# Performance work log

Measured on AMD Instinct MI355X. Metric: run time of the kernel, lower is better.

## Reference

```python
import jax, jax.numpy as jnp
import numpy as np

B, S, D = 2, 1024, 4096          # batch, prefill seqlen, model dim
H, KVH, HD = 32, 8, 128          # q heads, kv heads, head dim
MAX = 2048                       # kv-cache capacity
THETA = 1000000.0
REP = H // KVH


def _rope_tables(pos):
    # pos: [S] int -> cos/sin [S, HD]
    inv_freq = 1.0 / (THETA ** (jnp.arange(0, HD, 2, dtype=jnp.float32) / HD))
    freqs = pos[:, None].astype(jnp.float32) * inv_freq[None, :]
    emb = jnp.concatenate([freqs, freqs], axis=-1)
    return jnp.cos(emb), jnp.sin(emb)


def _rotate_half(t):
    t1, t2 = jnp.split(t, 2, axis=-1)
    return jnp.concatenate([-t2, t1], axis=-1)


def setup_inputs() -> dict:
    key = jax.random.key(0)
    k = jax.random.split(key, 8)
    sc = 1.0 / np.sqrt(D)
    x = jax.random.normal(k[0], (B, S, D), jnp.float32)
    storage_idx = jnp.arange(S, dtype=jnp.int32)
    cache = jnp.zeros((2, 1, B, KVH, MAX, HD), jnp.float32)
    causal = jnp.tril(jnp.ones((MAX, MAX), bool))
    mask = jnp.where(causal, 0.0, -1e9).astype(jnp.float32)
    Wq = jax.random.normal(k[1], (D, H * HD), jnp.float32) * sc
    bq = jax.random.normal(k[2], (H * HD,), jnp.float32) * 0.01
    Wk = jax.random.normal(k[3], (D, KVH * HD), jnp.float32) * sc
    bk = jax.random.normal(k[4], (KVH * HD,), jnp.float32) * 0.01
    Wv = jax.random.normal(k[5], (D, KVH * HD), jnp.float32) * sc
    bv = jax.random.normal(k[6], (KVH * HD,), jnp.float32) * 0.01
    Wo = jax.random.normal(k[7], (H * HD, D), jnp.float32) * sc
    return {"x": x, "storage_idx": storage_idx, "cache": cache, "mask": mask,
            "Wq": Wq, "bq": bq, "Wk": Wk, "bk": bk, "Wv": Wv, "bv": bv, "Wo": Wo}


def reference(x, storage_idx, cache, mask, Wq, bq, Wk, bk, Wv, bv, Wo):
    bsz, seqlen, _ = x.shape
    # QKV projections -> [b, heads, s, hd]
    xq = (x @ Wq + bq).reshape(bsz, seqlen, H, HD).transpose(0, 2, 1, 3)
    xk = (x @ Wk + bk).reshape(bsz, seqlen, KVH, HD).transpose(0, 2, 1, 3)
    xv = (x @ Wv + bv).reshape(bsz, seqlen, KVH, HD).transpose(0, 2, 1, 3)
    # inline RoPE at positions storage_idx
    cos, sin = _rope_tables(storage_idx)       # [s, hd]
    cos = cos[None, None]                      # [1,1,s,hd]
    sin = sin[None, None]
    xq = xq * cos + _rotate_half(xq) * sin
    xk = xk * cos + _rotate_half(xk) * sin
    # KV-cache scatter (index_copy_ on dim -2 at storage_idx)
    keys = cache[0, 0].at[:, :, storage_idx, :].set(xk)    # [b, kvh, MAX, hd]
    values = cache[1, 0].at[:, :, storage_idx, :].set(xv)
    # GQA: repeat kv heads
    keys = jnp.repeat(keys, REP, axis=1)       # [b, H, MAX, hd]
    values = jnp.repeat(values, REP, axis=1)
    # attention with additive mask rows gathered at storage_idx
    scores = jnp.einsum('bhqd,bhkd->bhqk', xq, keys) / np.sqrt(HD)
    scores = scores + mask[storage_idx][None, None]        # [b, H, s, MAX]
    attn = jax.nn.softmax(scores, axis=-1)
    out = jnp.einsum('bhqk,bhkd->bhqd', attn, values)
    out = out.transpose(0, 2, 1, 3).reshape(bsz, seqlen, H * HD)
    return out @ Wo
```

## Files before the change

kernel.cpp:

```cpp
#include <hip/hip_runtime.h>
#include <hip/hip_bf16.h>

typedef unsigned short u16;
typedef unsigned int   u32;
using bf16x8 = __attribute__((ext_vector_type(8))) short;
using f32x4  = __attribute__((ext_vector_type(4))) float;
using f32x16 = __attribute__((ext_vector_type(16))) float;

#define AS1 __attribute__((address_space(1)))
#define AS3 __attribute__((address_space(3)))

static constexpr int S_   = 1024;
static constexpr int D_   = 4096;
static constexpr int H_   = 32;
static constexpr int KVH_ = 8;
static constexpr int HD_  = 128;
static constexpr int NQKV = H_*HD_ + 2*KVH_*HD_;

__device__ __forceinline__ u16 f2bf(float f) {
  union { float f; u32 u; } v; v.f = f;
  u32 r = v.u + 0x7FFFu + ((v.u >> 16) & 1u);
  return (u16)(r >> 16);
}

__global__ void k_convert(const float* __restrict__ src, u16* __restrict__ dst, int n4) {
  int i = blockIdx.x * blockDim.x + threadIdx.x;
  if (i >= n4) return;
  float4 v = ((const float4*)src)[i];
  ushort4 o;
  o.x = f2bf(v.x); o.y = f2bf(v.y); o.z = f2bf(v.z); o.w = f2bf(v.w);
  ((ushort4*)dst)[i] = o;
}

__global__ __launch_bounds__(256) void k_transpose_all(
    const float* __restrict__ Wq, const float* __restrict__ Wk,
    const float* __restrict__ Wv, const float* __restrict__ Wo,
    u16* __restrict__ WB, u16* __restrict__ WoT) {
  constexpr int K = 4096;
  __shared__ float t[64][65];
  int id = blockIdx.x;
  const float* src; u16* dst; int N, tx, ty;
  if (id < 4096)      { src = Wq; dst = WB;                        N = 4096; tx = id & 63; ty = id >> 6; }
  else if (id < 5120) { id -= 4096; src = Wk; dst = WB + (size_t)4096*K; N = 1024; tx = id & 15; ty = id >> 4; }
  else if (id < 6144) { id -= 5120; src = Wv; dst = WB + (size_t)5120*K; N = 1024; tx = id & 15; ty = id >> 4; }
  else                { id -= 6144; src = Wo; dst = WoT;           N = 4096; tx = id & 63; ty = id >> 6; }
  int k0 = ty * 64, n0 = tx * 64;
  int tid = threadIdx.x;
  int lr = tid >> 4;
  int lc = (tid & 15) * 4;
#pragma unroll
  for (int i = 0; i < 4; ++i) {
    float4 v = *(const float4*)&src[(size_t)(k0 + lr + i*16) * N + n0 + lc];
    t[lc+0][lr + i*16] = v.x;
    t[lc+1][lr + i*16] = v.y;
    t[lc+2][lr + i*16] = v.z;
    t[lc+3][lr + i*16] = v.w;
  }
  __syncthreads();
  int wn = tid >> 3;
  int wk = (tid & 7) * 8;
#pragma unroll
  for (int i = 0; i < 2; ++i) {
    const float* row = &t[wn + i*32][wk];
    ushort4 a, b;
    a.x = f2bf(row[0]); a.y = f2bf(row[1]); a.z = f2bf(row[2]); a.w = f2bf(row[3]);
    b.x = f2bf(row[4]); b.y = f2bf(row[5]); b.z = f2bf(row[6]); b.w = f2bf(row[7]);
    u16* o = &dst[(size_t)(n0 + wn + i*32) * K + k0 + wk];
    *(ushort4*)o = a;
    *(ushort4*)(o + 4) = b;
  }
}

__global__ void k_transpose_v(const u16* __restrict__ src, u16* __restrict__ dst) {
  __shared__ u16 t[32][33];
  int bg = blockIdx.z;
  int s0 = blockIdx.x * 32, h0 = blockIdx.y * 32;
  src += (size_t)bg * S_ * HD_;
  dst += (size_t)bg * S_ * HD_;
  int tx = threadIdx.x, ty = threadIdx.y;
#pragma unroll
  for (int i = 0; i < 4; ++i)
    t[ty + i*8][tx] = src[(size_t)(s0 + ty + i*8) * HD_ + h0 + tx];
  __syncthreads();
#pragma unroll
  for (int i = 0; i < 4; ++i)
    dst[(size_t)(h0 + ty + i*8) * S_ + s0 + tx] = t[tx][ty + i*8];
}

__global__ void k_rope(const int* __restrict__ sidx, float* __restrict__ cosd,
                       float* __restrict__ sind) {
  int i = blockIdx.x * blockDim.x + threadIdx.x;
  int s = i >> 6, d = i & 63;
  float pos  = (float)sidx[s];
  float invf = expf(-0.21586735246819178f * (float)d);
  float ph   = pos * invf;
  cosd[i] = cosf(ph);
  sind[i] = sinf(ph);
}

#define BAR   __builtin_amdgcn_s_barrier()
#define SCHB  __builtin_amdgcn_sched_barrier(0)

__global__ __launch_bounds__(512, 2) void k_gemmq(
    const u16* __restrict__ A, const u16* __restrict__ Bt,
    const float* __restrict__ bq, const float* __restrict__ bk,
    const float* __restrict__ bv,
    const float* __restrict__ cosd, const float* __restrict__ sind,
    u16* __restrict__ qb, u16* __restrict__ kb, u16* __restrict__ vb)
{
  constexpr int K = 4096;
  constexpr int ABYT = 256*128, BBYT = 256*128, STEP = ABYT+BBYT;
  __shared__ __align__(16) char lds[2*STEP];

  const int cpx = (int)gridDim.x >> 3;
  const int wkid = ((int)blockIdx.x & 7)*cpx + ((int)blockIdx.x >> 3);
  const int NT = 24;
  const int m0 = (wkid / NT) * 256, n0 = (wkid % NT) * 256;
  const int tid = threadIdx.x, w = tid>>6, lane = tid&63;
  const int l15 = lane&15, l4 = lane>>4;
  const int wr = w>>1, wc = w&1;
  const int row0 = tid>>3;
  const int ss = (tid&7) ^ (row0&7);
  const int NK = K >> 6;

  f32x4 acc[4][8];
#pragma unroll
  for (int i = 0; i < 4; ++i)
#pragma unroll
    for (int j = 0; j < 8; ++j) acc[i][j] = (f32x4){0.f,0.f,0.f,0.f};

  bf16x8 af[2][2][2];
  bf16x8 bfr[2][4][2];

#define QCHUNK(kt_, part_, r0c_)                                              \
  __builtin_amdgcn_global_load_lds(                                           \
    (AS1 void*)(((part_) ? Bt + (size_t)(n0 + (r0c_) + row0)*K                \
                         : A  + (size_t)(m0 + (r0c_) + row0)*K)               \
                + (size_t)(kt_)*64 + ss*8),                                   \
    (AS3 void*)(lds + ((kt_)&1)*STEP + (part_)*ABYT + (r0c_)*128 + w*1024),   \
    16, 0, 0)

#define QR_A(mh_, lA_)                                                        \
  _Pragma("unroll") for (int i2 = 0; i2 < 2; ++i2)                            \
  _Pragma("unroll") for (int kk = 0; kk < 2; ++kk) {                          \
    int row = wr*64 + ((mh_)*2 + i2)*16 + l15;                                \
    af[mh_][i2][kk] = *(const bf16x8*)((lA_) + row*128 + (((kk*4+l4) ^ (row&7)) << 4)); }

#define QR_B(nh_, lB_)                                                        \
  _Pragma("unroll") for (int jj = 0; jj < 4; ++jj)                            \
  _Pragma("unroll") for (int kk = 0; kk < 2; ++kk) {                          \
    int row = wc*128 + ((nh_)*4 + jj)*16 + l15;                               \
    bfr[nh_][jj][kk] = *(const bf16x8*)((lB_) + row*128 + (((kk*4+l4) ^ (row&7)) << 4)); }

#define QMFMA(mh_, nh_)                                                       \
  __builtin_amdgcn_s_setprio(1);                                              \
  _Pragma("unroll") for (int i2 = 0; i2 < 2; ++i2)                            \
  _Pragma("unroll") for (int jj = 0; jj < 4; ++jj)                            \
  _Pragma("unroll") for (int kk = 0; kk < 2; ++kk)                            \
    acc[(mh_)*2+i2][(nh_)*4+jj] = __builtin_amdgcn_mfma_f32_16x16x32_bf16(    \
        af[mh_][i2][kk], bfr[nh_][jj][kk], acc[(mh_)*2+i2][(nh_)*4+jj], 0, 0, 0); \
  __builtin_amdgcn_s_setprio(0);

  QCHUNK(0,0,0); QCHUNK(0,0,64); QCHUNK(0,0,128); QCHUNK(0,0,192);
  QCHUNK(0,1,0); QCHUNK(0,1,64); QCHUNK(0,1,128); QCHUNK(0,1,192);
  QCHUNK(1,0,0); QCHUNK(1,0,64); QCHUNK(1,0,128); QCHUNK(1,0,192);
  QCHUNK(1,1,0); QCHUNK(1,1,64); QCHUNK(1,1,128); QCHUNK(1,1,192);
  asm volatile("s_waitcnt vmcnt(8)" ::: "memory");
  BAR; SCHB;
  {
    const char* lA0 = lds;
    const char* lB0 = lds + ABYT;
    QR_A(0, lA0); QR_B(0, lB0);
  }

  for (int kt = 0; kt < NK; ++kt) {
    const char* lA = lds + (kt&1)*STEP;
    const char* lB = lA + ABYT;
    QR_B(1, lB);
    asm volatile("s_waitcnt lgkmcnt(8)" ::: "memory");
    SCHB;
    QMFMA(0,0);
    QR_A(1, lA);
    asm volatile("s_waitcnt lgkmcnt(4)" ::: "memory");
    BAR; SCHB;
    if (kt+2 < NK) { QCHUNK(kt+2,1,0); QCHUNK(kt+2,1,64); QCHUNK(kt+2,1,128); QCHUNK(kt+2,1,192); }
    QMFMA(0,1);
    asm volatile("s_waitcnt lgkmcnt(0)" ::: "memory");
    BAR; SCHB;
    if (kt+2 < NK) { QCHUNK(kt+2,0,0); QCHUNK(kt+2,0,64); QCHUNK(kt+2,0,128); QCHUNK(kt+2,0,192); }
    QMFMA(1,0);
    if (kt+1 < NK) {
      if (kt+2 < NK) asm volatile("s_waitcnt vmcnt(8)" ::: "memory");
      else           asm volatile("s_waitcnt vmcnt(0)" ::: "memory");
      BAR; SCHB;
      const char* lAn = lds + ((kt+1)&1)*STEP;
      const char* lBn = lAn + ABYT;
      QR_A(0, lAn); QR_B(0, lBn);
      SCHB;
    }
    QMFMA(1,1);
  }
#undef QCHUNK
#undef QR_A
#undef QR_B
#undef QMFMA

  const int btype = (n0 >= H_*HD_) + (n0 >= H_*HD_ + KVH_*HD_);
  const int colbase = n0 + wc*128 - (btype==1 ? H_*HD_ : btype==2 ? H_*HD_+KVH_*HD_ : 0);
  const int hloc = colbase >> 7;
  const float* bias = btype==0 ? bq : btype==1 ? bk : bv;
  u16* dst = btype==0 ? qb : btype==1 ? kb : vb;
  const int nheads = btype==0 ? H_ : KVH_;
  const float scale = btype==0 ? 0.08838834764831845f : 1.0f;

  float bb[8];
#pragma unroll
  for (int j = 0; j < 8; ++j) bb[j] = bias[colbase + j*16 + l15];

#pragma unroll
  for (int i = 0; i < 4; ++i)
#pragma unroll
    for (int r = 0; r < 4; ++r) {
      int sr = m0 + wr*64 + i*16 + l4*4 + r;
      int b_ = sr >> 10, s_ = sr & 1023;
      size_t obase = (((size_t)b_*nheads + hloc)*S_ + s_)*(size_t)HD_;
      if (btype < 2) {
#pragma unroll
        for (int j = 0; j < 4; ++j) {
          float cs = cosd[s_*64 + j*16 + l15];
          float sn = sind[s_*64 + j*16 + l15];
          float lo = acc[i][j][r]   + bb[j];
          float hi = acc[i][j+4][r] + bb[j+4];
          dst[obase + j*16 + l15]      = f2bf((lo*cs - hi*sn) * scale);
          dst[obase + 64 + j*16 + l15] = f2bf((hi*cs + lo*sn) * scale);
        }
      } else {
#pragma unroll
        for (int j = 0; j < 8; ++j)
          dst[obase + j*16 + l15] = f2bf(acc[i][j][r] + bb[j]);
      }
    }
}

__global__ __launch_bounds__(512, 2) void k_gemmo(
    const u16* __restrict__ A, const u16* __restrict__ Bt,
    float* __restrict__ C, int N, int K)
{
  constexpr int ABYT = 128*128, BBYT = 256*128, STEP = ABYT+BBYT;
  __shared__ __align__(16) char lds[2*STEP];

  const int cpx = (int)gridDim.x >> 3;
  const int wkid = ((int)blockIdx.x & 7)*cpx + ((int)blockIdx.x >> 3);
  const int NT = N / 256;
  const int m0 = (wkid / NT) * 128, n0 = (wkid % NT) * 256;
  const int tid = threadIdx.x, w = tid>>6, lane = tid&63;
  const int l31 = lane & 31, lh = lane >> 5;
  const int wr = w>>2, wc = w&3;
  const int row0 = tid>>3;
  const int ss = (tid&7) ^ (row0&7);
  const int NK = K >> 6;

  f32x16 acc00 = {}, acc01 = {}, acc10 = {}, acc11 = {};

  bf16x8 af[2][4];
  bf16x8 bfr[2][4];

#define OCHUNK(kt_, part_, r0c_)                                              \
  __builtin_amdgcn_global_load_lds(                                           \
    (AS1 void*)(((part_) ? Bt + (size_t)(n0 + (r0c_) + row0)*K                \
                         : A  + (size_t)(m0 + (r0c_) + row0)*K)               \
                + (size_t)(kt_)*64 + ss*8),                                   \
    (AS3 void*)(lds + ((kt_)&1)*STEP + (part_)*ABYT + (r0c_)*128 + w*1024),   \
    16, 0, 0)

#define OR_A(mh_, lA_)                                                        \
  _Pragma("unroll") for (int st = 0; st < 4; ++st) {                          \
    int row = wr*64 + (mh_)*32 + l31;                                         \
    af[mh_][st] = *(const bf16x8*)((lA_) + row*128 + ((((st*2)+lh) ^ (row&7)) << 4)); }

#define OR_B(nh_, lB_)                                                        \
  _Pragma("unroll") for (int st = 0; st < 4; ++st) {                          \
    int row = wc*64 + (nh_)*32 + l31;                                         \
    bfr[nh_][st] = *(const bf16x8*)((lB_) + row*128 + ((((st*2)+lh) ^ (row&7)) << 4)); }

#define OMFMA(mh_, nh_, accv_)                                                \
  __builtin_amdgcn_s_setprio(1);                                              \
  _Pragma("unroll") for (int st = 0; st < 4; ++st)                            \
    accv_ = __builtin_amdgcn_mfma_f32_32x32x16_bf16(af[mh_][st], bfr[nh_][st], accv_, 0, 0, 0); \
  __builtin_amdgcn_s_setprio(0);

  OCHUNK(0,0,0); OCHUNK(0,0,64);
  OCHUNK(0,1,0); OCHUNK(0,1,64); OCHUNK(0,1,128); OCHUNK(0,1,192);
  OCHUNK(1,0,0); OCHUNK(1,0,64);
  OCHUNK(1,1,0); OCHUNK(1,1,64); OCHUNK(1,1,128); OCHUNK(1,1,192);
  asm volatile("s_waitcnt vmcnt(6)" ::: "memory");
  BAR; SCHB;
  {
    const char* lA0 = lds;
    const char* lB0 = lds + ABYT;
    OR_A(0, lA0); OR_B(0, lB0);
  }

  for (int kt = 0; kt < NK; ++kt) {
    const char* lA = lds + (kt&1)*STEP;
    const char* lB = lA + ABYT;
    OR_B(1, lB);
    asm volatile("s_waitcnt lgkmcnt(4)" ::: "memory");
    SCHB;
    OMFMA(0,0, acc00);
    OR_A(1, lA);
    asm volatile("s_waitcnt lgkmcnt(4)" ::: "memory");
    BAR; SCHB;
    if (kt+2 < NK) { OCHUNK(kt+2,1,0); OCHUNK(kt+2,1,64); OCHUNK(kt+2,1,128); OCHUNK(kt+2,1,192); }
    OMFMA(0,1, acc01);
    asm volatile("s_waitcnt lgkmcnt(0)" ::: "memory");
    BAR; SCHB;
    if (kt+2 < NK) { OCHUNK(kt+2,0,0); OCHUNK(kt+2,0,64); }
    OMFMA(1,0, acc10);
    if (kt+1 < NK) {
      if (kt+2 < NK) asm volatile("s_waitcnt vmcnt(6)" ::: "memory");
      else           asm volatile("s_waitcnt vmcnt(0)" ::: "memory");
      BAR; SCHB;
      const char* lAn = lds + ((kt+1)&1)*STEP;
      const char* lBn = lAn + ABYT;
      OR_A(0, lAn); OR_B(0, lBn);
      SCHB;
    }
    OMFMA(1,1, acc11);
  }
#undef OCHUNK
#undef OR_A
#undef OR_B
#undef OMFMA

#define OWRITE(mh_, nh_, accv_)                                               \
  _Pragma("unroll") for (int r = 0; r < 16; ++r) {                            \
    int row = m0 + wr*64 + (mh_)*32 + (r & 3) + 8*(r >> 2) + 4*lh;            \
    int col = n0 + wc*64 + (nh_)*32 + l31;                                    \
    C[(size_t)row * N + col] = accv_[r]; }
  OWRITE(0,0, acc00); OWRITE(0,1, acc01); OWRITE(1,0, acc10); OWRITE(1,1, acc11);
#undef OWRITE
}

__global__ __launch_bounds__(256, 4) void k_attn(
    const u16* __restrict__ Q, const u16* __restrict__ Kc,
    const u16* __restrict__ Vt, u16* __restrict__ AO)
{
  __shared__ __align__(16) char Kls[2][16384];
  __shared__ __align__(16) char Vls[2][16384];
  __shared__ u16 Pl[4][1024];

  int id = blockIdx.x;
  int slot = id >> 3;
  int bg   = (id & 7)*2 + (slot & 1);
  int rem  = slot >> 1;
  int h_in = rem & 3, bx = rem >> 2;
  int b = bg >> 3, g = bg & 7, h = g*4 + h_in;
  int tA = bx, tB = 15 - bx;

  int tid = threadIdx.x, w = tid >> 6, lane = tid & 63;
  int l15 = lane & 15, l4 = lane >> 4;
  const u16* Qh = Q  + ((size_t)b*H_   + h) * S_ * HD_;
  const u16* Kp = Kc + ((size_t)b*KVH_ + g) * S_ * HD_;
  const u16* Vp = Vt + ((size_t)b*KVH_ + g) * (size_t)HD_ * S_;
  u16* AOh = AO + ((size_t)b*S_) * (H_*HD_) + h*HD_;
  char* Pw = (char*)&Pl[w][0];

  int kOff[4], vOff[4];
#pragma unroll
  for (int c = 0; c < 4; ++c) {
    int ci = c*256 + tid;
    int krow = ci >> 4, ks = ci & 15;
    kOff[c] = krow * HD_ + ((ks & 8) | ((ks & 7) ^ (krow & 7))) * 8;
    int vrow = ci >> 3, vs = ci & 7;
    vOff[c] = vrow * S_ + (vs ^ (vrow & 7)) * 8;
  }

#define ASTAGE(kv_, bb_) {                                                    \
    const u16* ks_ = Kp + (size_t)(kv_) * 64 * HD_;                           \
    const u16* vs_ = Vp + (size_t)(kv_) * 64;                                 \
    _Pragma("unroll") for (int c = 0; c < 4; ++c) {                           \
      __builtin_amdgcn_global_load_lds((AS1 void*)(ks_ + kOff[c]),            \
          (AS3 void*)(&Kls[bb_][0] + c*4096 + w*1024), 16, 0, 0);             \
      __builtin_amdgcn_global_load_lds((AS1 void*)(vs_ + vOff[c]),            \
          (AS3 void*)(&Vls[bb_][0] + c*4096 + w*1024), 16, 0, 0); } }

  bf16x8 qf[4];
#pragma unroll
  for (int kc = 0; kc < 4; ++kc)
    qf[kc] = *(const bf16x8*)(Qh + (size_t)(tA*64 + w*16 + l15)*HD_ + kc*32 + l4*8);

  f32x4 o[8];
#pragma unroll
  for (int n = 0; n < 8; ++n) o[n] = (f32x4){0.f,0.f,0.f,0.f};
  float mrow[4] = {-3e38f,-3e38f,-3e38f,-3e38f};
  float lrow[4] = {0.f,0.f,0.f,0.f};

  ASTAGE(0, 0);
  asm volatile("s_waitcnt vmcnt(0)" ::: "memory");
  __builtin_amdgcn_s_barrier();

  const int NIT = tA + tB + 2;
  int buf = 0;
  for (int it = 0; it < NIT; ++it) {
    bool phA = (it <= tA);
    int kv = phA ? it : it - tA - 1;
    int qt = phA ? tA : tB;
    if (it + 1 < NIT) {
      int kvn = (it + 1 <= tA) ? it + 1 : it - tA;
      ASTAGE(kvn, buf ^ 1);
    }
    const char* Ksb = &Kls[buf][0];
    const char* Vsb = &Vls[buf][0];

    f32x4 sc[4];
    __builtin_amdgcn_s_setprio(1);
#pragma unroll
    for (int ct = 0; ct < 4; ++ct) {
      f32x4 s4 = (f32x4){0.f,0.f,0.f,0.f};
#pragma unroll
      for (int kc = 0; kc < 4; ++kc) {
        int row = ct*16 + l15, s = kc*4 + l4;
        bf16x8 kf = *(const bf16x8*)(Ksb + row*256 + ((((s & 7) ^ (row & 7)) | (s & 8)) << 4));
        s4 = __builtin_amdgcn_mfma_f32_16x16x32_bf16(qf[kc], kf, s4, 0, 0, 0);
      }
      sc[ct] = s4;
    }
    __builtin_amdgcn_s_setprio(0);

    if (kv == qt) {
      int qrow0 = qt*64 + w*16;
#pragma unroll
      for (int ct = 0; ct < 4; ++ct)
#pragma unroll
        for (int r = 0; r < 4; ++r) {
          int col = kv*64 + ct*16 + l15;
          if (col > qrow0 + l4*4 + r) sc[ct][r] = -1e9f;
        }
    }

    float f[4];
#pragma unroll
    for (int r = 0; r < 4; ++r) {
      float mx = fmaxf(fmaxf(sc[0][r], sc[1][r]), fmaxf(sc[2][r], sc[3][r]));
      mx = fmaxf(mx, __shfl_xor(mx, 1));
      mx = fmaxf(mx, __shfl_xor(mx, 2));
      mx = fmaxf(mx, __shfl_xor(mx, 4));
      mx = fmaxf(mx, __shfl_xor(mx, 8));
      float nm = fmaxf(mrow[r], mx);
      f[r] = __expf(mrow[r] - nm);
      mrow[r] = nm;
    }
    float rs[4] = {0.f,0.f,0.f,0.f};
#pragma unroll
    for (int ct = 0; ct < 4; ++ct)
#pragma unroll
      for (int r = 0; r < 4; ++r) {
        float p = __expf(sc[ct][r] - mrow[r]);
        rs[r] += p;
        int row = l4*4 + r, col = ct*16 + l15;
        int byte = row*128 + (((col >> 3) ^ (row & 7)) << 4) + (col & 7)*2;
        *(u16*)(Pw + byte) = f2bf(p);
      }
#pragma unroll
    for (int r = 0; r < 4; ++r) {
      float sum = rs[r];
      sum += __shfl_xor(sum, 1);
      sum += __shfl_xor(sum, 2);
      sum += __shfl_xor(sum, 4);
      sum += __shfl_xor(sum, 8);
      lrow[r] = lrow[r]*f[r] + sum;
    }
#pragma unroll
    for (int n = 0; n < 8; ++n)
#pragma unroll
      for (int r = 0; r < 4; ++r) o[n][r] *= f[r];

    __builtin_amdgcn_s_setprio(1);
#pragma unroll
    for (int kk = 0; kk < 2; ++kk) {
      int pbyte = l15*128 + (((kk*4 + l4) ^ (l15 & 7)) << 4);
      bf16x8 pf = *(const bf16x8*)(Pw + pbyte);
#pragma unroll
      for (int n = 0; n < 8; ++n) {
        int vrow = n*16 + l15, s = kk*4 + l4;
        bf16x8 vf = *(const bf16x8*)(Vsb + vrow*128 + ((s ^ (vrow & 7)) << 4));
        o[n] = __builtin_amdgcn_mfma_f32_16x16x32_bf16(pf, vf, o[n], 0, 0, 0);
      }
    }
    __builtin_amdgcn_s_setprio(0);

    if (it == tA) {
#pragma unroll
      for (int n = 0; n < 8; ++n)
#pragma unroll
        for (int r = 0; r < 4; ++r) {
          int srow = tA*64 + w*16 + l4*4 + r;
          AOh[(size_t)srow * (H_*HD_) + n*16 + l15] = f2bf(o[n][r] / lrow[r]);
        }
#pragma unroll
      for (int n = 0; n < 8; ++n) o[n] = (f32x4){0.f,0.f,0.f,0.f};
#pragma unroll
      for (int r = 0; r < 4; ++r) { mrow[r] = -3e38f; lrow[r] = 0.f; }
#pragma unroll
      for (int kc = 0; kc < 4; ++kc)
        qf[kc] = *(const bf16x8*)(Qh + (size_t)(tB*64 + w*16 + l15)*HD_ + kc*32 + l4*8);
    }

    asm volatile("s_waitcnt vmcnt(0)" ::: "memory");
    __builtin_amdgcn_s_barrier();
    buf ^= 1;
  }
#undef ASTAGE

#pragma unroll
  for (int n = 0; n < 8; ++n)
#pragma unroll
    for (int r = 0; r < 4; ++r) {
      int srow = tB*64 + w*16 + l4*4 + r;
      AOh[(size_t)srow * (H_*HD_) + n*16 + l15] = f2bf(o[n][r] / lrow[r]);
    }
}

extern "C" void kernel_launch(void* const* d_in, const int* in_sizes, int n_in,
                              void* d_out, int out_size, void* d_ws, size_t ws_size,
                              hipStream_t stream) {
  (void)in_sizes; (void)n_in; (void)out_size; (void)ws_size;
  const float* x   = (const float*)d_in[0];
  const int*   sid = (const int*)  d_in[1];
  const float* Wq  = (const float*)d_in[4];
  const float* bq  = (const float*)d_in[5];
  const float* Wk  = (const float*)d_in[6];
  const float* bk  = (const float*)d_in[7];
  const float* Wv  = (const float*)d_in[8];
  const float* bv  = (const float*)d_in[9];
  const float* Wo  = (const float*)d_in[10];
  float* out = (float*)d_out;

  char* ws = (char*)d_ws;
  u16*   xb   = (u16*)  (ws);
  u16*   WB   = (u16*)  (ws + 16777216);
  u16*   WoT  = (u16*)  (ws + 67108864);
  u16*   qb   = (u16*)  (ws + 150994944);
  u16*   kb   = (u16*)  (ws + 167772160);
  u16*   vb   = (u16*)  (ws + 171966464);
  u16*   VT   = (u16*)  (ws + 176160768);
  float* cosd = (float*)(ws + 180355072);
  float* sind = (float*)(ws + 180617216);
  u16*   AO   = xb;

  dim3 tb(32, 8);
  k_convert<<<8192, 256, 0, stream>>>(x, xb, (2048*4096)/4);
  k_transpose_all<<<10240, 256, 0, stream>>>(Wq, Wk, Wv, Wo, WB, WoT);
  k_rope<<<256, 256, 0, stream>>>(sid, cosd, sind);
  k_gemmq<<<192, 512, 0, stream>>>(xb, WB, bq, bk, bv, cosd, sind, qb, kb, vb);
  k_transpose_v<<<dim3(32,4,16), tb, 0, stream>>>(vb, VT);
  k_attn<<<512, 256, 0, stream>>>(qb, kb, VT, AO);
  k_gemmo<<<256, 512, 0, stream>>>(AO, WoT, out, 4096, 4096);
}
```

Measured before the change: 287.9 us.

## Retile QKV GEMM to 128x192 with 4 waves and permuted weight columns

Changes the fused QKV GEMM tile from 256x256 with 8 waves to 128x192 with 4 waves and 512 blocks, so the grid fills more of the 256 CUs instead of 192 blocks. Because 192 is not a multiple of the 128-wide head, the weight transpose now permutes Q/K columns so each pair of adjacent 16-column groups holds the matching lo/hi RoPE halves. That lets the epilogue apply RoPE within a single wave's tile. The smaller tile lowers arithmetic intensity per block and makes the epilogue indexing more complex.

```diff
diff --git a/kernel.cpp b/kernel.cpp
--- a/kernel.cpp
+++ b/kernel.cpp
@@ -39,18 +39,28 @@
   constexpr int K = 4096;
   __shared__ float t[64][65];
   int id = blockIdx.x;
-  const float* src; u16* dst; int N, tx, ty;
-  if (id < 4096)      { src = Wq; dst = WB;                        N = 4096; tx = id & 63; ty = id >> 6; }
-  else if (id < 5120) { id -= 4096; src = Wk; dst = WB + (size_t)4096*K; N = 1024; tx = id & 15; ty = id >> 4; }
-  else if (id < 6144) { id -= 5120; src = Wv; dst = WB + (size_t)5120*K; N = 1024; tx = id & 15; ty = id >> 4; }
-  else                { id -= 6144; src = Wo; dst = WoT;           N = 4096; tx = id & 63; ty = id >> 6; }
+  const float* src; u16* dst; int N, tx, ty, perm;
+  if (id < 4096)      { src = Wq; dst = WB;                        N = 4096; tx = id & 63; ty = id >> 6; perm = 1; }
+  else if (id < 5120) { id -= 4096; src = Wk; dst = WB + (size_t)4096*K; N = 1024; tx = id & 15; ty = id >> 4; perm = 1; }
+  else if (id < 6144) { id -= 5120; src = Wv; dst = WB + (size_t)5120*K; N = 1024; tx = id & 15; ty = id >> 4; perm = 0; }
+  else                { id -= 6144; src = Wo; dst = WoT;           N = 4096; tx = id & 63; ty = id >> 6; perm = 0; }
   int k0 = ty * 64, n0 = tx * 64;
   int tid = threadIdx.x;
+  int srcb[4];
+#pragma unroll
+  for (int g = 0; g < 4; ++g) {
+    int np = n0 + g*16;
+    if (perm) {
+      int f = (np >> 4) & 7, m = f >> 1;
+      srcb[g] = (np & ~127) + ((f & 1) ? 64 + m*16 : m*16);
+    } else srcb[g] = np;
+  }
   int lr = tid >> 4;
   int lc = (tid & 15) * 4;
+  int scol = srcb[lc >> 4] + (lc & 15);
 #pragma unroll
   for (int i = 0; i < 4; ++i) {
-    float4 v = *(const float4*)&src[(size_t)(k0 + lr + i*16) * N + n0 + lc];
+    float4 v = *(const float4*)&src[(size_t)(k0 + lr + i*16) * N + scol];
     t[lc+0][lr + i*16] = v.x;
     t[lc+1][lr + i*16] = v.y;
     t[lc+2][lr + i*16] = v.z;
@@ -101,7 +111,7 @@
 #define BAR   __builtin_amdgcn_s_barrier()
 #define SCHB  __builtin_amdgcn_sched_barrier(0)
 
-__global__ __launch_bounds__(512, 2) void k_gemmq(
+__global__ __launch_bounds__(256, 2) void k_gemmq(
     const u16* __restrict__ A, const u16* __restrict__ Bt,
     const float* __restrict__ bq, const float* __restrict__ bk,
     const float* __restrict__ bv,
@@ -109,13 +119,13 @@
     u16* __restrict__ qb, u16* __restrict__ kb, u16* __restrict__ vb)
 {
   constexpr int K = 4096;
-  constexpr int ABYT = 256*128, BBYT = 256*128, STEP = ABYT+BBYT;
+  constexpr int ABYT = 128*128, BBYT = 192*128, STEP = ABYT+BBYT;
   __shared__ __align__(16) char lds[2*STEP];
 
   const int cpx = (int)gridDim.x >> 3;
   const int wkid = ((int)blockIdx.x & 7)*cpx + ((int)blockIdx.x >> 3);
-  const int NT = 24;
-  const int m0 = (wkid / NT) * 256, n0 = (wkid % NT) * 256;
+  const int NT = 32;
+  const int m0 = (wkid / NT) * 128, n0 = (wkid % NT) * 192;
   const int tid = threadIdx.x, w = tid>>6, lane = tid&63;
   const int l15 = lane&15, l4 = lane>>4;
   const int wr = w>>1, wc = w&1;
@@ -123,14 +133,14 @@
   const int ss = (tid&7) ^ (row0&7);
   const int NK = K >> 6;
 
-  f32x4 acc[4][8];
+  f32x4 acc[4][6];
 #pragma unroll
   for (int i = 0; i < 4; ++i)
 #pragma unroll
-    for (int j = 0; j < 8; ++j) acc[i][j] = (f32x4){0.f,0.f,0.f,0.f};
+    for (int j = 0; j < 6; ++j) acc[i][j] = (f32x4){0.f,0.f,0.f,0.f};
 
   bf16x8 af[2][2][2];
-  bf16x8 bfr[2][4][2];
+  bf16x8 bfr[2][3][2];
 
 #define QCHUNK(kt_, part_, r0c_)                                              \
   __builtin_amdgcn_global_load_lds(                                           \
@@ -140,6 +150,10 @@
     (AS3 void*)(lds + ((kt_)&1)*STEP + (part_)*ABYT + (r0c_)*128 + w*1024),   \
     16, 0, 0)
 
+#define QSTAGE_A(kt_)  { QCHUNK(kt_,0,0); QCHUNK(kt_,0,32); QCHUNK(kt_,0,64); QCHUNK(kt_,0,96); }
+#define QSTAGE_B(kt_)  { QCHUNK(kt_,1,0); QCHUNK(kt_,1,32); QCHUNK(kt_,1,64); \
+                         QCHUNK(kt_,1,96); QCHUNK(kt_,1,128); QCHUNK(kt_,1,160); }
+
 #define QR_A(mh_, lA_)                                                        \
   _Pragma("unroll") for (int i2 = 0; i2 < 2; ++i2)                            \
   _Pragma("unroll") for (int kk = 0; kk < 2; ++kk) {                          \
@@ -147,25 +161,23 @@
     af[mh_][i2][kk] = *(const bf16x8*)((lA_) + row*128 + (((kk*4+l4) ^ (row&7)) << 4)); }
 
 #define QR_B(nh_, lB_)                                                        \
-  _Pragma("unroll") for (int jj = 0; jj < 4; ++jj)                            \
+  _Pragma("unroll") for (int jj = 0; jj < 3; ++jj)                            \
   _Pragma("unroll") for (int kk = 0; kk < 2; ++kk) {                          \
-    int row = wc*128 + ((nh_)*4 + jj)*16 + l15;                               \
+    int row = wc*96 + ((nh_)*3 + jj)*16 + l15;                                \
     bfr[nh_][jj][kk] = *(const bf16x8*)((lB_) + row*128 + (((kk*4+l4) ^ (row&7)) << 4)); }
 
 #define QMFMA(mh_, nh_)                                                       \
   __builtin_amdgcn_s_setprio(1);                                              \
   _Pragma("unroll") for (int i2 = 0; i2 < 2; ++i2)                            \
-  _Pragma("unroll") for (int jj = 0; jj < 4; ++jj)                            \
+  _Pragma("unroll") for (int jj = 0; jj < 3; ++jj)                            \
   _Pragma("unroll") for (int kk = 0; kk < 2; ++kk)                            \
-    acc[(mh_)*2+i2][(nh_)*4+jj] = __builtin_amdgcn_mfma_f32_16x16x32_bf16(    \
-        af[mh_][i2][kk], bfr[nh_][jj][kk], acc[(mh_)*2+i2][(nh_)*4+jj], 0, 0, 0); \
+    acc[(mh_)*2+i2][(nh_)*3+jj] = __builtin_amdgcn_mfma_f32_16x16x32_bf16(    \
+        af[mh_][i2][kk], bfr[nh_][jj][kk], acc[(mh_)*2+i2][(nh_)*3+jj], 0, 0, 0); \
   __builtin_amdgcn_s_setprio(0);
 
-  QCHUNK(0,0,0); QCHUNK(0,0,64); QCHUNK(0,0,128); QCHUNK(0,0,192);
-  QCHUNK(0,1,0); QCHUNK(0,1,64); QCHUNK(0,1,128); QCHUNK(0,1,192);
-  QCHUNK(1,0,0); QCHUNK(1,0,64); QCHUNK(1,0,128); QCHUNK(1,0,192);
-  QCHUNK(1,1,0); QCHUNK(1,1,64); QCHUNK(1,1,128); QCHUNK(1,1,192);
-  asm volatile("s_waitcnt vmcnt(8)" ::: "memory");
+  QSTAGE_A(0); QSTAGE_B(0);
+  QSTAGE_A(1); QSTAGE_B(1);
+  asm volatile("s_waitcnt vmcnt(10)" ::: "memory");
   BAR; SCHB;
   {
     const char* lA0 = lds;
@@ -177,20 +189,20 @@
     const char* lA = lds + (kt&1)*STEP;
     const char* lB = lA + ABYT;
     QR_B(1, lB);
-    asm volatile("s_waitcnt lgkmcnt(8)" ::: "memory");
+    asm volatile("s_waitcnt lgkmcnt(6)" ::: "memory");
     SCHB;
     QMFMA(0,0);
     QR_A(1, lA);
     asm volatile("s_waitcnt lgkmcnt(4)" ::: "memory");
     BAR; SCHB;
-    if (kt+2 < NK) { QCHUNK(kt+2,1,0); QCHUNK(kt+2,1,64); QCHUNK(kt+2,1,128); QCHUNK(kt+2,1,192); }
+    if (kt+2 < NK) QSTAGE_B(kt+2);
     QMFMA(0,1);
     asm volatile("s_waitcnt lgkmcnt(0)" ::: "memory");
     BAR; SCHB;
-    if (kt+2 < NK) { QCHUNK(kt+2,0,0); QCHUNK(kt+2,0,64); QCHUNK(kt+2,0,128); QCHUNK(kt+2,0,192); }
+    if (kt+2 < NK) QSTAGE_A(kt+2);
     QMFMA(1,0);
     if (kt+1 < NK) {
-      if (kt+2 < NK) asm volatile("s_waitcnt vmcnt(8)" ::: "memory");
+      if (kt+2 < NK) asm volatile("s_waitcnt vmcnt(10)" ::: "memory");
       else           asm volatile("s_waitcnt vmcnt(0)" ::: "memory");
       BAR; SCHB;
       const char* lAn = lds + ((kt+1)&1)*STEP;
@@ -201,45 +213,58 @@
     QMFMA(1,1);
   }
 #undef QCHUNK
+#undef QSTAGE_A
+#undef QSTAGE_B
 #undef QR_A
 #undef QR_B
 #undef QMFMA
 
-  const int btype = (n0 >= H_*HD_) + (n0 >= H_*HD_ + KVH_*HD_);
-  const int colbase = n0 + wc*128 - (btype==1 ? H_*HD_ : btype==2 ? H_*HD_+KVH_*HD_ : 0);
-  const int hloc = colbase >> 7;
-  const float* bias = btype==0 ? bq : btype==1 ? bk : bv;
-  u16* dst = btype==0 ? qb : btype==1 ? kb : vb;
-  const int nheads = btype==0 ? H_ : KVH_;
-  const float scale = btype==0 ? 0.08838834764831845f : 1.0f;
-
-  float bb[8];
-#pragma unroll
-  for (int j = 0; j < 8; ++j) bb[j] = bias[colbase + j*16 + l15];
-
-#pragma unroll
-  for (int i = 0; i < 4; ++i)
-#pragma unroll
-    for (int r = 0; r < 4; ++r) {
-      int sr = m0 + wr*64 + i*16 + l4*4 + r;
-      int b_ = sr >> 10, s_ = sr & 1023;
-      size_t obase = (((size_t)b_*nheads + hloc)*S_ + s_)*(size_t)HD_;
-      if (btype < 2) {
-#pragma unroll
-        for (int j = 0; j < 4; ++j) {
-          float cs = cosd[s_*64 + j*16 + l15];
-          float sn = sind[s_*64 + j*16 + l15];
-          float lo = acc[i][j][r]   + bb[j];
-          float hi = acc[i][j+4][r] + bb[j+4];
-          dst[obase + j*16 + l15]      = f2bf((lo*cs - hi*sn) * scale);
-          dst[obase + 64 + j*16 + l15] = f2bf((hi*cs + lo*sn) * scale);
+  const int cb16 = (n0 + wc*96) >> 4;
+#pragma unroll
+  for (int p = 0; p < 3; ++p) {
+    int g0 = cb16 + 2*p;
+    if (g0 < 320) {
+      bool isQ = (g0 < 256);
+      int gs = isQ ? g0 : g0 - 256;
+      int h = gs >> 3, m = (gs & 7) >> 1;
+      int dlo = m*16 + l15;
+      const float* bias = isQ ? bq : bk;
+      u16* dst = isQ ? qb : kb;
+      int nheads = isQ ? H_ : KVH_;
+      float scale = isQ ? 0.08838834764831845f : 1.0f;
+      float b_lo = bias[h*128 + dlo];
+      float b_hi = bias[h*128 + 64 + dlo];
+#pragma unroll
+      for (int i = 0; i < 4; ++i)
+#pragma unroll
+        for (int r = 0; r < 4; ++r) {
+          int sr = m0 + wr*64 + i*16 + l4*4 + r;
+          int b_ = sr >> 10, s_ = sr & 1023;
+          float cs = cosd[s_*64 + dlo], sn = sind[s_*64 + dlo];
+          float lo = acc[i][2*p][r]   + b_lo;
+          float hi = acc[i][2*p+1][r] + b_hi;
+          size_t obase = (((size_t)b_*nheads + h)*S_ + s_)*(size_t)HD_;
+          dst[obase + dlo]      = f2bf((lo*cs - hi*sn) * scale);
+          dst[obase + 64 + dlo] = f2bf((hi*cs + lo*sn) * scale);
         }
-      } else {
-#pragma unroll
-        for (int j = 0; j < 8; ++j)
-          dst[obase + j*16 + l15] = f2bf(acc[i][j][r] + bb[j]);
+    } else {
+#pragma unroll
+      for (int q = 0; q < 2; ++q) {
+        int gv = g0 + q - 320;
+        int h = gv >> 3, d = (gv & 7)*16 + l15;
+        float bbv = bv[h*128 + d];
+#pragma unroll
+        for (int i = 0; i < 4; ++i)
+#pragma unroll
+          for (int r = 0; r < 4; ++r) {
+            int sr = m0 + wr*64 + i*16 + l4*4 + r;
+            int b_ = sr >> 10, s_ = sr & 1023;
+            size_t obase = (((size_t)b_*KVH_ + h)*S_ + s_)*(size_t)HD_;
+            vb[obase + d] = f2bf(acc[i][2*p+q][r] + bbv);
+          }
       }
     }
+  }
 }
 
 __global__ __launch_bounds__(512, 2) void k_gemmo(
@@ -553,7 +578,7 @@
   k_convert<<<8192, 256, 0, stream>>>(x, xb, (2048*4096)/4);
   k_transpose_all<<<10240, 256, 0, stream>>>(Wq, Wk, Wv, Wo, WB, WoT);
   k_rope<<<256, 256, 0, stream>>>(sid, cosd, sind);
-  k_gemmq<<<192, 512, 0, stream>>>(xb, WB, bq, bk, bv, cosd, sind, qb, kb, vb);
+  k_gemmq<<<512, 256, 0, stream>>>(xb, WB, bq, bk, bv, cosd, sind, qb, kb, vb);
   k_transpose_v<<<dim3(32,4,16), tb, 0, stream>>>(vb, VT);
   k_attn<<<512, 256, 0, stream>>>(qb, kb, VT, AO);
   k_gemmo<<<256, 512, 0, stream>>>(AO, WoT, out, 4096, 4096);
```

Result: slower. 310.5 us (+7.8%).
